# Kernel optimization log

Hardware: AMD Instinct MI355X
Metric: run time of the kernel (lower is better)

The kernel has to match this reference:

```python
import jax, jax.numpy as jnp
import numpy as np

DIM = 1024
HEADS = 16
DIM_HEAD = 64
DEPTH = 12
LN_EPS = 1e-5


def setup_inputs() -> dict:
    key = jax.random.key(0)
    k1, k2, k3 = jax.random.split(key, 3)
    B, N = 4, 2048
    inner = HEADS * DIM_HEAD
    x = jax.random.normal(k1, (B, N, DIM), dtype=jnp.float32)
    ln_w = jnp.ones((DIM,), jnp.float32)
    ln_b = jnp.zeros((DIM,), jnp.float32)
    w_qkv = jax.random.normal(k2, (DIM, 3 * inner), jnp.float32) * (DIM ** -0.5)
    w_out = jax.random.normal(k3, (inner, DIM), jnp.float32) * (inner ** -0.5)
    b_out = jnp.zeros((DIM,), jnp.float32)
    return {"x": x, "ln_w": ln_w, "ln_b": ln_b, "w_qkv": w_qkv,
            "w_out": w_out, "b_out": b_out, "layer_index": 2}


def reference(x, ln_w, ln_b, w_qkv, w_out, b_out, layer_index):
    B, N, D = x.shape
    scale = DIM_HEAD ** -0.5
    # LayerNorm
    mu = jnp.mean(x, axis=-1, keepdims=True)
    var = jnp.mean(jnp.square(x - mu), axis=-1, keepdims=True)
    xn = (x - mu) * jax.lax.rsqrt(var + LN_EPS) * ln_w + ln_b
    # QKV projection (no bias), split heads: b n (h d) -> b h n d
    qkv = xn @ w_qkv  # [B, N, 3*H*Dh]
    q, k, v = jnp.split(qkv, 3, axis=-1)
    def heads(t):
        return t.reshape(B, N, HEADS, DIM_HEAD).transpose(0, 2, 1, 3)
    q, k, v = heads(q), heads(k), heads(v)
    dots = jnp.einsum('bhnd,bhmd->bhnm', q, k) * scale  # [B,H,N,N]
    if layer_index < DEPTH // 2:
        attn = jax.nn.relu(dots)
    else:
        attn = jax.nn.softmax(dots, axis=-1)
    attn = attn / N  # divide by x.shape[1]
    out = jnp.einsum('bhnm,bhmd->bhnd', attn, v)
    out = out.transpose(0, 2, 1, 3).reshape(B, N, HEADS * DIM_HEAD)
    # to_out (heads > 1): Linear + (inactive) dropout
    return out @ w_out + b_out
```

## Files before the change

### kernel.cpp

```cpp
#include <hip/hip_runtime.h>
#include <stdint.h>

typedef __bf16 bf16x8 __attribute__((ext_vector_type(8)));
typedef __bf16 bf16x4 __attribute__((ext_vector_type(4)));
typedef float f32x4 __attribute__((ext_vector_type(4)));
typedef float f32x16 __attribute__((ext_vector_type(16)));

#define PSCALE (0.125f / 2048.0f)

#define GLOAD16(src, dst)                                                      \
  __builtin_amdgcn_global_load_lds(                                            \
      (__attribute__((address_space(1))) void*)const_cast<__bf16*>(src),       \
      (__attribute__((address_space(3))) void*)(dst), 16, 0, 0)

__global__ __launch_bounds__(256) void prep(
    const float* __restrict__ x, const float* __restrict__ lw,
    const float* __restrict__ lb, __bf16* __restrict__ xn,
    const float* __restrict__ w_qkv, __bf16* __restrict__ Wt1,
    const float* __restrict__ w_out, __bf16* __restrict__ Wt2) {
  __shared__ __bf16 T[64][72];
  __shared__ float red[8];
  const int b = blockIdx.x;
  const int t = threadIdx.x;
  if (b < 8192) {
    const float4 v = ((const float4*)(x + (size_t)b * 1024))[t];
    float s = v.x + v.y + v.z + v.w;
    float ss = v.x * v.x + v.y * v.y + v.z * v.z + v.w * v.w;
#pragma unroll
    for (int o = 32; o; o >>= 1) {
      s += __shfl_down(s, o);
      ss += __shfl_down(ss, o);
    }
    if ((t & 63) == 0) {
      red[t >> 6] = s;
      red[4 + (t >> 6)] = ss;
    }
    __syncthreads();
    const float tot = red[0] + red[1] + red[2] + red[3];
    const float tot2 = red[4] + red[5] + red[6] + red[7];
    const float mu = tot * (1.0f / 1024.0f);
    const float var = tot2 * (1.0f / 1024.0f) - mu * mu;
    const float rs = rsqrtf(var + 1e-5f);
    const float4 wv = ((const float4*)lw)[t];
    const float4 bv = ((const float4*)lb)[t];
    bf16x4 o;
    o[0] = (__bf16)((v.x - mu) * rs * wv.x + bv.x);
    o[1] = (__bf16)((v.y - mu) * rs * wv.y + bv.y);
    o[2] = (__bf16)((v.z - mu) * rs * wv.z + bv.z);
    o[3] = (__bf16)((v.w - mu) * rs * wv.w + bv.w);
    ((bf16x4*)xn)[(size_t)b * 256 + t] = o;
    return;
  }
  const float* A;
  __bf16* At;
  int R, C, bx, by;
  if (b < 8960) {
    const int ti = b - 8192;
    A = w_qkv; At = Wt1; R = 1024; C = 3072;
    bx = ti % 48; by = ti / 48;
  } else {
    const int ti = b - 8960;
    A = w_out; At = Wt2; R = 1024; C = 1024;
    bx = ti % 16; by = ti / 16;
  }
  const int rb = by * 64, cb = bx * 64;
  const int r = t >> 2, cg = t & 3;
#pragma unroll
  for (int k = 0; k < 4; ++k) {
    const float4 v =
        *(const float4*)(A + (size_t)(rb + r) * C + cb + cg * 16 + k * 4);
    T[cg * 16 + k * 4 + 0][r] = (__bf16)v.x;
    T[cg * 16 + k * 4 + 1][r] = (__bf16)v.y;
    T[cg * 16 + k * 4 + 2][r] = (__bf16)v.z;
    T[cg * 16 + k * 4 + 3][r] = (__bf16)v.w;
  }
  __syncthreads();
#pragma unroll
  for (int i = 0; i < 2; ++i) {
    const int j = i * 256 + t;
    const int c = j >> 3, s8 = j & 7;
    const bf16x8 o = *(const bf16x8*)&T[c][s8 * 8];
    *(bf16x8*)(At + (size_t)(cb + c) * R + rb + s8 * 8) = o;
  }
}

template <int MODE>
__global__ __launch_bounds__(512) void gemm_nt(
    const __bf16* __restrict__ A, const __bf16* __restrict__ B, int K,
    float* __restrict__ outF, __bf16* __restrict__ Qo, __bf16* __restrict__ Ko,
    __bf16* __restrict__ Vto, const float* __restrict__ bias) {
  __shared__ __bf16 Sm[3 * 24576];
  const int tid = threadIdx.x;
  const int lane = tid & 63, w = tid >> 6;
  const int g = lane >> 4, c15 = lane & 15;
  const int wr = w >> 2, wc = w & 3;
  const int linear = blockIdx.y * gridDim.x + blockIdx.x;
  const int per = (gridDim.x * gridDim.y) >> 3;
  const int nl = (linear & 7) * per + (linear >> 3);
  const int rb = (nl / gridDim.x) * 128, cb = (nl % gridDim.x) * 256;

  const __bf16* aSp[2];
  const __bf16* bSp[4];
  int aDo[2], bDo[4];
#pragma unroll
  for (int i = 0; i < 2; ++i) {
    const int j = i * 512 + tid, row = j >> 3, slot = j & 7;
    aSp[i] = A + (size_t)(rb + row) * K + ((slot ^ (row & 7)) << 3);
    aDo[i] = i * 4096 + w * 512;
  }
#pragma unroll
  for (int i = 0; i < 4; ++i) {
    const int j = i * 512 + tid, col = j >> 3, slot = j & 7;
    bSp[i] = B + (size_t)(cb + col) * K + ((slot ^ (col & 7)) << 3);
    bDo[i] = 8192 + i * 4096 + w * 512;
  }

  f32x4 acc[4][4] = {};
  const int nkb = K >> 6;

#pragma unroll
  for (int t = 0; t < 2; ++t) {
    __bf16* dst = Sm + t * 24576;
#pragma unroll
    for (int i = 0; i < 2; ++i) GLOAD16(aSp[i] + t * 64, dst + aDo[i]);
#pragma unroll
    for (int i = 0; i < 4; ++i) GLOAD16(bSp[i] + t * 64, dst + bDo[i]);
  }

  int cur = 0, stg = 2, koff = 128;
  for (int kb = 0; kb < nkb; ++kb) {
    if (kb == nkb - 1) {
      asm volatile("s_waitcnt vmcnt(0)" ::: "memory");
    } else {
      asm volatile("s_waitcnt vmcnt(6)" ::: "memory");
    }
    __builtin_amdgcn_s_barrier();
    const bool do_stage = (kb < nkb - 2);
    __bf16* sdst = Sm + stg * 24576;
    if (do_stage) {
#pragma unroll
      for (int i = 0; i < 2; ++i) GLOAD16(aSp[i] + koff, sdst + aDo[i]);
    }
    const __bf16* __restrict__ Ac = Sm + cur * 24576;
    const __bf16* __restrict__ Bc = Ac + 8192;
    {
      bf16x8 af[4], bfr[4];
      const int kc = g;
#pragma unroll
      for (int rt = 0; rt < 4; ++rt) {
        const int lr = wr * 64 + rt * 16 + c15;
        af[rt] = *(const bf16x8*)(Ac + lr * 64 + ((kc ^ (lr & 7)) << 3));
      }
#pragma unroll
      for (int ct = 0; ct < 4; ++ct) {
        const int lc = wc * 64 + ct * 16 + c15;
        bfr[ct] = *(const bf16x8*)(Bc + lc * 64 + ((kc ^ (lc & 7)) << 3));
      }
      __builtin_amdgcn_s_setprio(1);
#pragma unroll
      for (int rt = 0; rt < 4; ++rt)
#pragma unroll
        for (int ct = 0; ct < 4; ++ct)
          acc[rt][ct] = __builtin_amdgcn_mfma_f32_16x16x32_bf16(
              af[rt], bfr[ct], acc[rt][ct], 0, 0, 0);
      __builtin_amdgcn_s_setprio(0);
    }
    if (do_stage) {
#pragma unroll
      for (int i = 0; i < 4; ++i) GLOAD16(bSp[i] + koff, sdst + bDo[i]);
      koff += 64;
    }
    {
      bf16x8 af[4], bfr[4];
      const int kc = 4 + g;
#pragma unroll
      for (int rt = 0; rt < 4; ++rt) {
        const int lr = wr * 64 + rt * 16 + c15;
        af[rt] = *(const bf16x8*)(Ac + lr * 64 + ((kc ^ (lr & 7)) << 3));
      }
#pragma unroll
      for (int ct = 0; ct < 4; ++ct) {
        const int lc = wc * 64 + ct * 16 + c15;
        bfr[ct] = *(const bf16x8*)(Bc + lc * 64 + ((kc ^ (lc & 7)) << 3));
      }
      __builtin_amdgcn_s_setprio(1);
#pragma unroll
      for (int rt = 0; rt < 4; ++rt)
#pragma unroll
        for (int ct = 0; ct < 4; ++ct)
          acc[rt][ct] = __builtin_amdgcn_mfma_f32_16x16x32_bf16(
              af[rt], bfr[ct], acc[rt][ct], 0, 0, 0);
      __builtin_amdgcn_s_setprio(0);
    }
    cur = (cur == 2) ? 0 : cur + 1;
    stg = (stg == 2) ? 0 : stg + 1;
  }
  const int r00 = rb + wr * 64 + g * 4;
  if (MODE == 1) {
#pragma unroll
    for (int ct = 0; ct < 4; ++ct) {
      const int col = cb + wc * 64 + ct * 16 + c15;
      const float bv = bias[col];
#pragma unroll
      for (int rt = 0; rt < 4; ++rt) {
        const int row = r00 + rt * 16;
#pragma unroll
        for (int r = 0; r < 4; ++r)
          outF[(size_t)(row + r) * 1024 + col] = acc[rt][ct][r] + bv;
      }
    }
  } else {
#pragma unroll
    for (int ct = 0; ct < 4; ++ct) {
      const int col = cb + wc * 64 + ct * 16 + c15;
      const int part = col >> 10, rem = col & 1023;
      const int h = rem >> 6, d = rem & 63;
#pragma unroll
      for (int rt = 0; rt < 4; ++rt) {
        const int row = r00 + rt * 16;
        const int bi = row >> 11, n = row & 2047;
        const size_t bh = (size_t)bi * 16 + h;
        if (part == 2) {
          bf16x4 pv;
#pragma unroll
          for (int r = 0; r < 4; ++r) pv[r] = (__bf16)acc[rt][ct][r];
          *(bf16x4*)(Vto + (bh * 64 + d) * 2048 + n) = pv;
        } else if (part == 0) {
          __bf16* dst = Qo + (bh * 2048 + n) * 64 + d;
#pragma unroll
          for (int r = 0; r < 4; ++r)
            dst[(size_t)r * 64] = (__bf16)(acc[rt][ct][r] * PSCALE);
        } else {
          __bf16* dst = Ko + (bh * 2048 + n) * 64 + d;
#pragma unroll
          for (int r = 0; r < 4; ++r) dst[(size_t)r * 64] = (__bf16)acc[rt][ct][r];
        }
      }
    }
  }
}

__global__ __launch_bounds__(256, 2) void attn_relu(
    const __bf16* __restrict__ Q, const __bf16* __restrict__ K,
    const __bf16* __restrict__ Vt, __bf16* __restrict__ O) {
  __shared__ __bf16 Ks[2][128 * 64];
  __shared__ __bf16 Vs[2][64 * 128];
  const int tid = threadIdx.x;
  const int lane = tid & 63, wv = tid >> 6;
  const int hi = lane >> 5, c31 = lane & 31;
  const int bh = blockIdx.x, qb = blockIdx.y;
  const __bf16* Qg = Q + ((size_t)bh * 2048 + qb * 256) * 64;
  const __bf16* Kg = K + (size_t)bh * 2048 * 64;
  const __bf16* Vg = Vt + (size_t)bh * 64 * 2048;

  const __bf16* kp[4];
  const __bf16* vp[4];
#pragma unroll
  for (int i = 0; i < 4; ++i) {
    const int j = i * 256 + tid;
    const int X = j >> 3, s = j & 7;
    const int KX = (X & ~12) | ((X & 4) << 1) | ((X & 8) >> 1);
    kp[i] = Kg + (size_t)KX * 64 + ((s ^ (X & 7)) << 3);
    const int d = j >> 4, sl = j & 15;
    vp[i] = Vg + (size_t)d * 2048 + ((sl ^ (d & 15)) << 3);
  }
  const int dstoff = wv * 512;

  bf16x8 qf[2][4];
#pragma unroll
  for (int qg = 0; qg < 2; ++qg)
#pragma unroll
    for (int dw = 0; dw < 4; ++dw)
      qf[qg][dw] = *(const bf16x8*)(Qg + (wv * 64 + qg * 32 + c31) * 64 +
                                    dw * 16 + hi * 8);
  f32x16 oacc[2][2] = {};

#pragma unroll
  for (int i = 0; i < 4; ++i) GLOAD16(kp[i], Ks[0] + i * 2048 + dstoff);
#pragma unroll
  for (int i = 0; i < 4; ++i) GLOAD16(vp[i], Vs[0] + i * 2048 + dstoff);

  for (int kb = 0; kb < 16; ++kb) {
    const int cur = kb & 1;
    if (kb < 15) {
      const int nxt = cur ^ 1;
      const int ko = (kb + 1) * 8192, vo = (kb + 1) * 128;
#pragma unroll
      for (int i = 0; i < 4; ++i)
        GLOAD16(kp[i] + ko, Ks[nxt] + i * 2048 + dstoff);
#pragma unroll
      for (int i = 0; i < 4; ++i)
        GLOAD16(vp[i] + vo, Vs[nxt] + i * 2048 + dstoff);
      asm volatile("s_waitcnt vmcnt(8)" ::: "memory");
    } else {
      asm volatile("s_waitcnt vmcnt(0)" ::: "memory");
    }
    __builtin_amdgcn_s_barrier();
    const __bf16* __restrict__ Kc = Ks[cur];
    const __bf16* __restrict__ Vc = Vs[cur];
#pragma unroll
    for (int kb32 = 0; kb32 < 4; ++kb32) {
      bf16x8 kf[4];
      const int R = kb32 * 32 + c31;
#pragma unroll
      for (int dw = 0; dw < 4; ++dw)
        kf[dw] =
            *(const bf16x8*)(Kc + R * 64 + (((2 * dw + hi) ^ (R & 7)) << 3));
      f32x16 s[2] = {{}, {}};
      __builtin_amdgcn_s_setprio(1);
#pragma unroll
      for (int dw = 0; dw < 4; ++dw)
#pragma unroll
        for (int qg = 0; qg < 2; ++qg)
          s[qg] = __builtin_amdgcn_mfma_f32_32x32x16_bf16(kf[dw], qf[qg][dw],
                                                          s[qg], 0, 0, 0);
      __builtin_amdgcn_s_setprio(0);
      bf16x8 pa[2][2];
#pragma unroll
      for (int qg = 0; qg < 2; ++qg)
#pragma unroll
        for (int wl = 0; wl < 2; ++wl)
#pragma unroll
          for (int e = 0; e < 8; ++e)
            pa[qg][wl][e] = (__bf16)fmaxf(s[qg][8 * wl + e], 0.0f);
      __builtin_amdgcn_s_setprio(1);
#pragma unroll
      for (int wl = 0; wl < 2; ++wl) {
        const int win = 2 * kb32 + wl;
#pragma unroll
        for (int dc = 0; dc < 2; ++dc) {
          const int d = dc * 32 + c31;
          const bf16x8 vb = *(const bf16x8*)(
              Vc + d * 128 + (((2 * win + hi) ^ (d & 15)) << 3));
#pragma unroll
          for (int qg = 0; qg < 2; ++qg)
            oacc[qg][dc] = __builtin_amdgcn_mfma_f32_32x32x16_bf16(
                pa[qg][wl], vb, oacc[qg][dc], 0, 0, 0);
        }
      }
      __builtin_amdgcn_s_setprio(0);
    }
    __builtin_amdgcn_s_barrier();
  }
  const int bi = bh >> 4, h = bh & 15;
#pragma unroll
  for (int qg = 0; qg < 2; ++qg)
#pragma unroll
    for (int dc = 0; dc < 2; ++dc) {
      const int col = h * 64 + dc * 32 + c31;
#pragma unroll
      for (int r = 0; r < 16; ++r) {
        const int q = wv * 64 + qg * 32 + (r & 3) + 8 * (r >> 2) + 4 * hi;
        const int n0 = qb * 256 + q;
        O[((size_t)bi * 2048 + n0) * 1024 + col] = (__bf16)oacc[qg][dc][r];
      }
    }
}

extern "C" void kernel_launch(void* const* d_in, const int* in_sizes, int n_in,
                              void* d_out, int out_size, void* d_ws,
                              size_t ws_size, hipStream_t stream) {
  (void)in_sizes; (void)n_in; (void)out_size; (void)ws_size;
  const float* x = (const float*)d_in[0];
  const float* ln_w = (const float*)d_in[1];
  const float* ln_b = (const float*)d_in[2];
  const float* w_qkv = (const float*)d_in[3];
  const float* w_out = (const float*)d_in[4];
  const float* b_out = (const float*)d_in[5];
  char* ws = (char*)d_ws;
  __bf16* xn = (__bf16*)(ws);
  __bf16* Wt1 = (__bf16*)(ws + (size_t)(16u << 20));
  __bf16* Wt2 = (__bf16*)(ws + (size_t)(22u << 20));
  __bf16* Qb = (__bf16*)(ws + (size_t)(24u << 20));
  __bf16* Kb = (__bf16*)(ws + (size_t)(40u << 20));
  __bf16* Vtb = (__bf16*)(ws + (size_t)(56u << 20));
  __bf16* Ob = (__bf16*)(ws + (size_t)(72u << 20));
  float* out = (float*)d_out;

  prep<<<9216, 256, 0, stream>>>(x, ln_w, ln_b, xn, w_qkv, Wt1, w_out, Wt2);
  gemm_nt<0><<<dim3(12, 64), 512, 0, stream>>>(xn, Wt1, 1024, nullptr, Qb, Kb,
                                               Vtb, nullptr);
  attn_relu<<<dim3(64, 8), 256, 0, stream>>>(Qb, Kb, Vtb, Ob);
  gemm_nt<1><<<dim3(4, 64), 512, 0, stream>>>(Ob, Wt2, 1024, out, nullptr,
                                              nullptr, nullptr, b_out);
}
```

Baseline: 169.4 us.

## Split KV range across wave pairs in attention and reduce partial outputs in LDS

The attention kernel now handles 128 queries per block instead of 256 and launches twice as many blocks. Each pair of waves shares 64 queries and splits every 128-key tile between its two waves, so the partial outputs are summed through LDS at the end. Double-buffered async prefetch is replaced by a single buffer with a full wait each iteration. The LDS swizzle gains an extra XOR term. The aim is more parallelism and occupancy across the GPU, at the cost of an exposed load latency on every tile and an extra reduction step.

```diff
diff --git a/kernel.cpp b/kernel.cpp
--- a/kernel.cpp
+++ b/kernel.cpp
@@ -240,16 +240,17 @@
   }
 }
 
-__global__ __launch_bounds__(256, 2) void attn_relu(
+__global__ __launch_bounds__(256) void attn_relu(
     const __bf16* __restrict__ Q, const __bf16* __restrict__ K,
     const __bf16* __restrict__ Vt, __bf16* __restrict__ O) {
-  __shared__ __bf16 Ks[2][128 * 64];
-  __shared__ __bf16 Vs[2][64 * 128];
+  __shared__ __align__(16) float redF[8192];
+  __bf16* Sb = (__bf16*)redF;
   const int tid = threadIdx.x;
   const int lane = tid & 63, wv = tid >> 6;
   const int hi = lane >> 5, c31 = lane & 31;
+  const int pair = wv >> 1, half = wv & 1;
   const int bh = blockIdx.x, qb = blockIdx.y;
-  const __bf16* Qg = Q + ((size_t)bh * 2048 + qb * 256) * 64;
+  const __bf16* Qg = Q + ((size_t)bh * 2048 + qb * 128 + pair * 64) * 64;
   const __bf16* Kg = K + (size_t)bh * 2048 * 64;
   const __bf16* Vg = Vt + (size_t)bh * 64 * 2048;
 
@@ -260,9 +261,9 @@
     const int j = i * 256 + tid;
     const int X = j >> 3, s = j & 7;
     const int KX = (X & ~12) | ((X & 4) << 1) | ((X & 8) >> 1);
-    kp[i] = Kg + (size_t)KX * 64 + ((s ^ (X & 7)) << 3);
+    kp[i] = Kg + (size_t)KX * 64 + ((s ^ (X & 7) ^ ((X >> 3) & 3)) << 3);
     const int d = j >> 4, sl = j & 15;
-    vp[i] = Vg + (size_t)d * 2048 + ((sl ^ (d & 15)) << 3);
+    vp[i] = Vg + (size_t)d * 2048 + ((sl ^ (d & 15) ^ ((d >> 3) & 3)) << 3);
   }
   const int dstoff = wv * 512;
 
@@ -271,58 +272,44 @@
   for (int qg = 0; qg < 2; ++qg)
 #pragma unroll
     for (int dw = 0; dw < 4; ++dw)
-      qf[qg][dw] = *(const bf16x8*)(Qg + (wv * 64 + qg * 32 + c31) * 64 +
-                                    dw * 16 + hi * 8);
+      qf[qg][dw] =
+          *(const bf16x8*)(Qg + (qg * 32 + c31) * 64 + dw * 16 + hi * 8);
   f32x16 oacc[2][2] = {};
 
-#pragma unroll
-  for (int i = 0; i < 4; ++i) GLOAD16(kp[i], Ks[0] + i * 2048 + dstoff);
-#pragma unroll
-  for (int i = 0; i < 4; ++i) GLOAD16(vp[i], Vs[0] + i * 2048 + dstoff);
-
   for (int kb = 0; kb < 16; ++kb) {
-    const int cur = kb & 1;
-    if (kb < 15) {
-      const int nxt = cur ^ 1;
-      const int ko = (kb + 1) * 8192, vo = (kb + 1) * 128;
-#pragma unroll
-      for (int i = 0; i < 4; ++i)
-        GLOAD16(kp[i] + ko, Ks[nxt] + i * 2048 + dstoff);
-#pragma unroll
-      for (int i = 0; i < 4; ++i)
-        GLOAD16(vp[i] + vo, Vs[nxt] + i * 2048 + dstoff);
-      asm volatile("s_waitcnt vmcnt(8)" ::: "memory");
-    } else {
-      asm volatile("s_waitcnt vmcnt(0)" ::: "memory");
-    }
+#pragma unroll
+    for (int i = 0; i < 4; ++i)
+      GLOAD16(kp[i] + kb * 8192, Sb + i * 2048 + dstoff);
+#pragma unroll
+    for (int i = 0; i < 4; ++i)
+      GLOAD16(vp[i] + kb * 128, Sb + 8192 + i * 2048 + dstoff);
+    asm volatile("s_waitcnt vmcnt(0)" ::: "memory");
     __builtin_amdgcn_s_barrier();
-    const __bf16* __restrict__ Kc = Ks[cur];
-    const __bf16* __restrict__ Vc = Vs[cur];
-#pragma unroll
-    for (int kb32 = 0; kb32 < 4; ++kb32) {
+#pragma unroll
+    for (int sub = 0; sub < 2; ++sub) {
+      const int kb32 = 2 * half + sub;
+      const int R = kb32 * 32 + c31;
       bf16x8 kf[4];
-      const int R = kb32 * 32 + c31;
 #pragma unroll
       for (int dw = 0; dw < 4; ++dw)
-        kf[dw] =
-            *(const bf16x8*)(Kc + R * 64 + (((2 * dw + hi) ^ (R & 7)) << 3));
-      f32x16 s[2] = {{}, {}};
-      __builtin_amdgcn_s_setprio(1);
-#pragma unroll
-      for (int dw = 0; dw < 4; ++dw)
-#pragma unroll
-        for (int qg = 0; qg < 2; ++qg)
-          s[qg] = __builtin_amdgcn_mfma_f32_32x32x16_bf16(kf[dw], qf[qg][dw],
-                                                          s[qg], 0, 0, 0);
-      __builtin_amdgcn_s_setprio(0);
-      bf16x8 pa[2][2];
-#pragma unroll
-      for (int qg = 0; qg < 2; ++qg)
+        kf[dw] = *(const bf16x8*)(
+            Sb + R * 64 + (((2 * dw + hi) ^ (R & 7) ^ ((R >> 3) & 3)) << 3));
+      bf16x8 p[2][2];
+#pragma unroll
+      for (int qg = 0; qg < 2; ++qg) {
+        f32x16 s = {};
+        __builtin_amdgcn_s_setprio(1);
+#pragma unroll
+        for (int dw = 0; dw < 4; ++dw)
+          s = __builtin_amdgcn_mfma_f32_32x32x16_bf16(kf[dw], qf[qg][dw], s,
+                                                      0, 0, 0);
+        __builtin_amdgcn_s_setprio(0);
 #pragma unroll
         for (int wl = 0; wl < 2; ++wl)
 #pragma unroll
           for (int e = 0; e < 8; ++e)
-            pa[qg][wl][e] = (__bf16)fmaxf(s[qg][8 * wl + e], 0.0f);
+            p[qg][wl][e] = (__bf16)fmaxf(s[8 * wl + e], 0.0f);
+      }
       __builtin_amdgcn_s_setprio(1);
 #pragma unroll
       for (int wl = 0; wl < 2; ++wl) {
@@ -331,30 +318,61 @@
         for (int dc = 0; dc < 2; ++dc) {
           const int d = dc * 32 + c31;
           const bf16x8 vb = *(const bf16x8*)(
-              Vc + d * 128 + (((2 * win + hi) ^ (d & 15)) << 3));
-#pragma unroll
-          for (int qg = 0; qg < 2; ++qg)
-            oacc[qg][dc] = __builtin_amdgcn_mfma_f32_32x32x16_bf16(
-                pa[qg][wl], vb, oacc[qg][dc], 0, 0, 0);
+              Sb + 8192 + d * 128 +
+              (((2 * win + hi) ^ (d & 15) ^ ((d >> 3) & 3)) << 3));
+          oacc[0][dc] = __builtin_amdgcn_mfma_f32_32x32x16_bf16(
+              p[0][wl], vb, oacc[0][dc], 0, 0, 0);
+          oacc[1][dc] = __builtin_amdgcn_mfma_f32_32x32x16_bf16(
+              p[1][wl], vb, oacc[1][dc], 0, 0, 0);
         }
       }
       __builtin_amdgcn_s_setprio(0);
     }
     __builtin_amdgcn_s_barrier();
   }
-  const int bi = bh >> 4, h = bh & 15;
-#pragma unroll
-  for (int qg = 0; qg < 2; ++qg)
-#pragma unroll
-    for (int dc = 0; dc < 2; ++dc) {
-      const int col = h * 64 + dc * 32 + c31;
-#pragma unroll
-      for (int r = 0; r < 16; ++r) {
-        const int q = wv * 64 + qg * 32 + (r & 3) + 8 * (r >> 2) + 4 * hi;
-        const int n0 = qb * 256 + q;
-        O[((size_t)bi * 2048 + n0) * 1024 + col] = (__bf16)oacc[qg][dc][r];
-      }
-    }
+  if (half) {
+#pragma unroll
+    for (int qg = 0; qg < 2; ++qg)
+#pragma unroll
+      for (int dc = 0; dc < 2; ++dc)
+#pragma unroll
+        for (int r4 = 0; r4 < 4; ++r4) {
+          f32x4 t;
+#pragma unroll
+          for (int j = 0; j < 4; ++j) t[j] = oacc[qg][dc][r4 * 4 + j];
+          *(f32x4*)(redF + pair * 4096 + (qg * 2 + dc) * 1024 + r4 * 256 +
+                    lane * 4) = t;
+        }
+  }
+  __builtin_amdgcn_s_barrier();
+  if (!half) {
+#pragma unroll
+    for (int qg = 0; qg < 2; ++qg)
+#pragma unroll
+      for (int dc = 0; dc < 2; ++dc)
+#pragma unroll
+        for (int r4 = 0; r4 < 4; ++r4) {
+          const f32x4 t = *(const f32x4*)(redF + pair * 4096 +
+                                          (qg * 2 + dc) * 1024 + r4 * 256 +
+                                          lane * 4);
+#pragma unroll
+          for (int j = 0; j < 4; ++j) oacc[qg][dc][r4 * 4 + j] += t[j];
+        }
+    const int bi = bh >> 4, h = bh & 15;
+#pragma unroll
+    for (int qg = 0; qg < 2; ++qg)
+#pragma unroll
+      for (int dc = 0; dc < 2; ++dc) {
+        const int col = h * 64 + dc * 32 + c31;
+#pragma unroll
+        for (int r = 0; r < 16; ++r) {
+          const int q =
+              pair * 64 + qg * 32 + (r & 3) + 8 * (r >> 2) + 4 * hi;
+          const int n0 = qb * 128 + q;
+          O[((size_t)bi * 2048 + n0) * 1024 + col] = (__bf16)oacc[qg][dc][r];
+        }
+      }
+  }
 }
 
 extern "C" void kernel_launch(void* const* d_in, const int* in_sizes, int n_in,
@@ -380,7 +398,7 @@
   prep<<<9216, 256, 0, stream>>>(x, ln_w, ln_b, xn, w_qkv, Wt1, w_out, Wt2);
   gemm_nt<0><<<dim3(12, 64), 512, 0, stream>>>(xn, Wt1, 1024, nullptr, Qb, Kb,
                                                Vtb, nullptr);
-  attn_relu<<<dim3(64, 8), 256, 0, stream>>>(Qb, Kb, Vtb, Ob);
+  attn_relu<<<dim3(64, 16), 256, 0, stream>>>(Qb, Kb, Vtb, Ob);
   gemm_nt<1><<<dim3(4, 64), 512, 0, stream>>>(Ob, Wt2, 1024, out, nullptr,
                                               nullptr, nullptr, b_out);
 }
```

Measured after the change: 182.3 us. 7.6% more time.
